# Optimization experiments

Measured on AMD Instinct MI355X. Metric: run time of the kernel, lower is better.

The kernel has to match this reference:

```python
import jax, jax.numpy as jnp
import numpy as np

N, S, T = 32, 256, 256
ENC, H, MEL, PRE, DIN, PN = 512, 256, 80, 128, 64, 512


def setup_inputs():
    key = jax.random.key(0)
    ks = iter(jax.random.split(key, 64))
    def rn(shape, s=0.05):
        return jax.random.normal(next(ks), shape, dtype=jnp.float32) * s
    return dict(
        encoder_outputs=rn((N, S, ENC), 1.0),
        mels=rn((N, MEL, T), 1.0),
        text_lengths=jax.random.randint(next(ks), (N,), 1, S),
        output_lengths=jax.random.randint(next(ks), (N,), 1, T),
        tf_ratio=0,
        enc_Wih=rn((2, 2, 4 * H, ENC)), enc_Whh=rn((2, 2, 4 * H, H)), enc_b=rn((2, 2, 4 * H)),
        Wk=rn((512, 512, 9)), bk=rn((512,)), Wv=rn((512, 512, 9)), bv=rn((512,)),
        Wq=rn((512, 64, 24)), bq=rn((512,)),
        initial_context=rn((1, 1, MEL), 1.0),
        pre_W1=rn((PRE, MEL), 0.1), pre_b1=rn((PRE,)), pre_s1=jnp.ones(PRE, jnp.float32),
        pre_W2=rn((PRE, PRE), 0.1), pre_b2=rn((PRE,)), pre_s2=jnp.ones(PRE, jnp.float32),
        pre_W3=rn((DIN, PRE), 0.1), pre_b3=rn((DIN,)),
        proj_W=rn((DIN, 512)), proj_b=rn((DIN,)),
        gamma=jnp.full((1,), 0.5, jnp.float32),
        dec_Wih0=rn((4 * H, DIN)), dec_Wih_rest=rn((3, 4 * H, H)), dec_Whh=rn((4, 4 * H, H)), dec_b=rn((4, 4 * H)),
        fc_W=rn((MEL, H), 0.1), fc_b=rn((MEL,)),
        stop_W=rn((1, 2 * H), 0.1), stop_b=rn((1,)),
        pn_W0=rn((PN, MEL, 5), 0.1), pn_b0=rn((PN,)),
        pn_Wmid=rn((3, PN, PN, 5)), pn_bmid=rn((3, PN)),
        pn_W4=rn((MEL, PN, 5)), pn_b4=rn((MEL,)),
        pn_bn_scale=jnp.ones((4, PN), jnp.float32), pn_bn_bias=jnp.zeros((4, PN), jnp.float32),
        pn_bn_scale_out=jnp.ones((MEL,), jnp.float32), pn_bn_bias_out=jnp.zeros((MEL,), jnp.float32),
        psine_w=jnp.ones((4, PN), jnp.float32),
    )


def _lstm_scan(xs, Wih, Whh, b, reverse=False):
    # xs: [T, N, D]; torch gate order (i, f, g, o); b = b_ih + b_hh combined
    n = xs.shape[1]
    h0 = jnp.zeros((n, Whh.shape[1]), xs.dtype)
    def step(carry, x):
        h, c = carry
        i, f, g, o = jnp.split(x @ Wih.T + h @ Whh.T + b, 4, axis=-1)
        c = jax.nn.sigmoid(f) * c + jax.nn.sigmoid(i) * jnp.tanh(g)
        h = jax.nn.sigmoid(o) * jnp.tanh(c)
        return (h, c), h
    (h, c), ys = jax.lax.scan(step, (h0, h0), xs, reverse=reverse)
    return ys, h, c


def _conv1d(x, w, b, pad):
    y = jax.lax.conv_general_dilated(x, w, (1,), [pad], dimension_numbers=('NCH', 'OIH', 'NCH'))
    return y + b[None, :, None]


def reference(encoder_outputs, mels, text_lengths, output_lengths, tf_ratio,
              enc_Wih, enc_Whh, enc_b, Wk, bk, Wv, bv, Wq, bq, initial_context,
              pre_W1, pre_b1, pre_s1, pre_W2, pre_b2, pre_s2, pre_W3, pre_b3,
              proj_W, proj_b, gamma, dec_Wih0, dec_Wih_rest, dec_Whh, dec_b,
              fc_W, fc_b, stop_W, stop_b, pn_W0, pn_b0, pn_Wmid, pn_bmid,
              pn_W4, pn_b4, pn_bn_scale, pn_bn_bias, pn_bn_scale_out, pn_bn_bias_out, psine_w):
    # ---- bidirectional 2-layer encoder LSTM ----
    x = encoder_outputs.transpose(1, 0, 2)  # [S, N, ENC]
    hs, cs = [], []
    for l in range(2):
        yf, hf, cf = _lstm_scan(x, enc_Wih[l, 0], enc_Whh[l, 0], enc_b[l, 0])
        yb, hb, cb = _lstm_scan(x, enc_Wih[l, 1], enc_Whh[l, 1], enc_b[l, 1], reverse=True)
        x = jnp.concatenate([yf, yb], -1)
        hs += [hf, hb]; cs += [cf, cb]
    h0 = jnp.stack(hs); c0 = jnp.stack(cs)      # [4, N, H]  (l0f,l0b,l1f,l1b)
    enc_fwd_hidden = hs[2]                       # hidden[-2] = layer1 forward
    enc_nct = x.transpose(1, 2, 0)               # [N, 512, S]
    # ---- K/V conv attention map ----
    k = _conv1d(enc_nct, Wk, bk, (0, 0))         # [N, 512, S-8]
    v = _conv1d(enc_nct, Wv, bv, (0, 0))
    a = jax.nn.softmax(jnp.einsum('nck,ndk->ncd', k, v), axis=-1)  # [N, 512, 512]
    # ---- teacher-forced inputs (tf_ratio == 0 -> rand(1) > 0 always) ----
    mels_ntc = mels.transpose(0, 2, 1)           # [N, T, MEL]
    nb, nt = mels_ntc.shape[0], mels_ntc.shape[1]
    teacher = jnp.concatenate([jnp.tile(initial_context, (nb, 1, 1)), mels_ntc], 1)[:, :nt]
    # prenet (eval: dropout off); PSine: sin(x) * w
    p = jnp.sin(teacher @ pre_W1.T + pre_b1) * pre_s1
    p = jnp.sin(p @ pre_W2.T + pre_b2) * pre_s2
    context = p @ pre_W3.T + pre_b3              # [N, T, 64]
    # ---- growing-context Q conv: at step i, output position i of the
    # kernel-24 pad-12 conv over context[:, :i+1] only involves kernel taps
    # 0..12 (taps 13..23 index positions > i which are zero padding), so it
    # equals a causal conv with the first 13 taps and left pad 12. ----
    q = _conv1d(context.transpose(0, 2, 1), Wq[:, :, :13], bq, (12, 0))  # [N, 512, T]
    o = jnp.einsum('ncd,ndt->ntc', a, q)         # [N, T, 512]
    dec_in = context + gamma * (o @ proj_W.T + proj_b)  # [N, T, 64]
    # ---- 4-layer decoder LSTM (eval: inter-layer dropout off) ----
    def dec_step(carry, xt):
        h, c = carry
        inp = xt
        nh, nc = [], []
        for l in range(4):
            Wih = dec_Wih0 if l == 0 else dec_Wih_rest[l - 1]
            i, f, g, oo = jnp.split(inp @ Wih.T + h[l] @ dec_Whh[l].T + dec_b[l], 4, axis=-1)
            cl = jax.nn.sigmoid(f) * c[l] + jax.nn.sigmoid(i) * jnp.tanh(g)
            hl = jax.nn.sigmoid(oo) * jnp.tanh(cl)
            nh.append(hl); nc.append(cl); inp = hl
        return (jnp.stack(nh), jnp.stack(nc)), inp
    _, top = jax.lax.scan(dec_step, (h0, c0), dec_in.transpose(1, 0, 2))  # [T, N, H]
    outputs = (top @ fc_W.T + fc_b).transpose(1, 2, 0)                    # [N, MEL, T]
    stop_in = jnp.concatenate([top, jnp.broadcast_to(enc_fwd_hidden, top.shape)], -1)
    stop_tokens = (stop_in @ stop_W.T + stop_b).transpose(1, 0, 2)        # [N, T, 1]
    # ---- postnet (eval: BN is per-channel affine, dropout off) ----
    y = _conv1d(outputs, pn_W0, pn_b0, (2, 2))
    y = jnp.sin(y * pn_bn_scale[0][None, :, None] + pn_bn_bias[0][None, :, None]) * psine_w[0][None, :, None]
    for i in range(3):
        y = _conv1d(y, pn_Wmid[i], pn_bmid[i], (2, 2))
        y = jnp.sin(y * pn_bn_scale[i + 1][None, :, None] + pn_bn_bias[i + 1][None, :, None]) * psine_w[i + 1][None, :, None]
    y = _conv1d(y, pn_W4, pn_b4, (2, 2))
    y = y * pn_bn_scale_out[None, :, None] + pn_bn_bias_out[None, :, None]
    post_preds = y + outputs
    return (outputs, post_preds, stop_tokens)
```

## Files before the change

### kernel.cpp

```cpp
#include <hip/hip_runtime.h>
#include <hip/hip_bf16.h>

typedef __hip_bfloat16 bf16;
#define DEV __device__ __forceinline__

typedef __attribute__((ext_vector_type(8))) short bfrag;
typedef __attribute__((ext_vector_type(4))) float facc;

#define PG_    0L
#define ABUF_  0L
#define DPG0_  8388608L
#define Y0_    16777216L
#define ENCT_  18874368L
#define KB_    20975872L
#define VB_    23073024L
#define ABF_   25170176L
#define TEA_   29364480L
#define P1_    29757696L
#define P2_    30281984L
#define CTXP_  30806272L
#define CTXL_  31080704L
#define QB_    31342848L
#define OB_    33440000L
#define DIN_   35537152L
#define TOP_   35799296L
#define OUTF_  36847872L
#define OUTT_  37503232L
#define PN1_   37902592L
#define PN2_   40032512L
#define WKT_   42162432L
#define WVT_   43342080L
#define WQT_   44521728L
#define W1P_   44734720L
#define PN0T_  44740864L
#define PNMT_  44863744L
#define PN4T_  46829824L
#define HDEC_  46964992L
#define HFIN_  47030528L
#define CFIN_  47063296L
#define FLAG_  47096320L
#define CVT_   47096336L
#define WS_NEED_BYTES (52092992L * 4L)

DEV float b2f(bf16 x) { return __bfloat162float(x); }
DEV bf16  f2b(float x) { return __float2bfloat16(x); }
DEV float flo(unsigned v) { union { unsigned u; float f; } c; c.u = v << 16; return c.f; }
DEV float fhi(unsigned v) { union { unsigned u; float f; } c; c.u = v & 0xffff0000u; return c.f; }
DEV unsigned bu(bf16 x) { union { bf16 b; unsigned short u; } c; c.b = x; return (unsigned)c.u; }
DEV unsigned pk2(float a, float b) { return bu(f2b(a)) | (bu(f2b(b)) << 16); }
DEV float sigm(float x) { return 1.0f / (1.0f + __expf(-x)); }

DEV void spin_ge(unsigned* f, unsigned tgt) {
  while (__hip_atomic_load(f, __ATOMIC_RELAXED, __HIP_MEMORY_SCOPE_AGENT) < tgt)
    __builtin_amdgcn_s_sleep(2);
}

DEV void acc8(float& a, uint4 w, const float* x) {
  a += flo(w.x) * x[0] + fhi(w.x) * x[1] + flo(w.y) * x[2] + fhi(w.y) * x[3]
     + flo(w.z) * x[4] + fhi(w.z) * x[5] + flo(w.w) * x[6] + fhi(w.w) * x[7];
}

__global__ void k_flag(const unsigned short* psw, unsigned* flag) {
  if (threadIdx.x == 0 && blockIdx.x == 0) *flag = (psw[0] != 0) ? 1u : 0u;
}

__global__ void k_cvt(const void* src, bf16* dst, long n, const unsigned* flag) {
  long i = (long)blockIdx.x * 256 + threadIdx.x;
  const long stride = (long)gridDim.x * 256;
  if (*flag) {
    const bf16* s = (const bf16*)src;
    for (; i < n; i += stride) dst[i] = s[i];
  } else {
    const float* s = (const float*)src;
    for (; i < n; i += stride) dst[i] = f2b(s[i]);
  }
}

enum { ACT_NONE = 0, ACT_BIAS = 1, ACT_PSINE = 2, ACT_POSTNET = 3, ACT_DECIN = 4, ACT_RESADD = 5 };
enum { SM_F32 = 0, SM_BF16 = 1, SM_PADROW = 2, SM_NCT = 3, SM_TNF32 = 4, SM_RESOUT = 5 };

struct GP {
  const bf16* A; const bf16* B;
  long az, bz, btap;
  int M, N, K, taps;
  int rshift, rpitch;
  float* Cf; bf16* Cb;
  long cz; int cld;
  int p2, pad2, tmax, tp;
  const bf16* bias; long biasz;
  const bf16* s1; const bf16* s2; const bf16* s3;
  const bf16* aux; int auxld;
  const bf16* gamma; const float* res;
};

template<int SM, int ACTM>
__global__ __launch_bounds__(256) void k_gemm(GP p) {
  __shared__ bf16 As[64][40];
  __shared__ bf16 Bs[64][40];
  const int tid = threadIdx.x;
  const int z = blockIdx.z;
  const bf16* Ab = p.A + (long)z * p.az;
  const bf16* Bb = p.B + (long)z * p.bz;
  const int m0 = blockIdx.x * 64, c0 = blockIdx.y * 64;
  const int w = tid >> 6, l = tid & 63;
  const int lrow = tid & 63, lk = (tid >> 6) * 8;
  facc acc[4];
  #pragma unroll
  for (int s = 0; s < 4; ++s) acc[s] = facc{0.f, 0.f, 0.f, 0.f};
  const int am = m0 + lrow;
  const int grp = am >> p.rshift;
  const long arowbase = (long)grp * p.rpitch + (am - (grp << p.rshift));
  const int brow = c0 + lrow;
  const bool bok = brow < p.N;
  const int arow_f = w * 16 + (l & 15);
  const int kf = (l >> 4) * 8;
  for (int j = 0; j < p.taps; ++j) {
    const bf16* Aj = Ab + (arowbase + j) * (long)p.K + lk;
    const bf16* Bj = Bb + (long)j * p.btap + (long)brow * p.K + lk;
    for (int k0 = 0; k0 < p.K; k0 += 32) {
      __syncthreads();
      {
        uint4 av = *(const uint4*)(Aj + k0);
        *(uint4*)&As[lrow][lk] = av;
        uint4 bvv; bvv.x = bvv.y = bvv.z = bvv.w = 0u;
        if (bok) bvv = *(const uint4*)(Bj + k0);
        *(uint4*)&Bs[lrow][lk] = bvv;
      }
      __syncthreads();
      bfrag af = *(const bfrag*)&As[arow_f][kf];
      #pragma unroll
      for (int s = 0; s < 4; ++s) {
        bfrag bf = *(const bfrag*)&Bs[s * 16 + (l & 15)][kf];
        acc[s] = __builtin_amdgcn_mfma_f32_16x16x32_bf16(af, bf, acc[s], 0, 0, 0);
      }
    }
  }
  float gf = 0.f;
  if constexpr (ACTM == ACT_DECIN) gf = b2f(p.gamma[0]);
  #pragma unroll
  for (int s = 0; s < 4; ++s) {
    const int c = c0 + s * 16 + (l & 15);
    if (c >= p.N) continue;
    #pragma unroll
    for (int i = 0; i < 4; ++i) {
      const int m = m0 + w * 16 + ((l >> 4) << 2) + i;
      const int n_ = m >> 8, t_ = m & 255;
      float x = acc[s][i];
      if constexpr (ACTM == ACT_BIAS) x += b2f(p.bias[(long)z * p.biasz + c]);
      else if constexpr (ACTM == ACT_PSINE) x = sinf(x + b2f(p.bias[c])) * b2f(p.s1[c]);
      else if constexpr (ACTM == ACT_POSTNET) x = sinf((x + b2f(p.bias[c])) * b2f(p.s1[c]) + b2f(p.s2[c])) * b2f(p.s3[c]);
      else if constexpr (ACTM == ACT_DECIN) x = b2f(p.aux[(long)m * p.auxld + c]) + gf * (x + b2f(p.bias[c]));
      else if constexpr (ACTM == ACT_RESADD) x = (x + b2f(p.bias[c])) * b2f(p.s1[c]) + b2f(p.s2[c]);
      if constexpr (SM == SM_F32) p.Cf[(long)z * p.cz + (long)m * p.cld + c] = x;
      else if constexpr (SM == SM_BF16) p.Cb[(long)z * p.cz + (long)m * p.cld + c] = f2b(x);
      else if constexpr (SM == SM_PADROW) p.Cb[((long)n_ * p.p2 + p.pad2 + t_) * (long)p.cld + c] = f2b(x);
      else if constexpr (SM == SM_NCT) { if (t_ < p.tmax) p.Cb[((long)n_ * p.p2 + c) * (long)p.tp + t_] = f2b(x); }
      else if constexpr (SM == SM_TNF32) { const int nn = m & 31, tt = m >> 5; p.Cf[((long)nn * p.p2 + c) * (long)p.tp + tt] = x; }
      else if constexpr (SM == SM_RESOUT) { const long off = ((long)n_ * p.p2 + c) * (long)p.tp + t_; p.Cf[off] = x + p.res[off]; }
    }
  }
}

__global__ void k_wtr2(const bf16* __restrict__ in, bf16* __restrict__ out) {
  long i = (long)blockIdx.x * 256 + threadIdx.x;
  if (i >= 524288L) return;
  int jj = (int)(i & 7);
  int r = (int)((i >> 3) & 1023);
  int k8 = (int)((i >> 13) & 31);
  int d = (int)(i >> 18);
  out[i] = in[((long)d * 1024 + r) * 256 + k8 * 8 + jj];
}

__global__ __launch_bounds__(256) void k_enc_scan(
    const float* __restrict__ pg,
    const bf16* __restrict__ WT,
    bf16* __restrict__ ycat,
    float* __restrict__ hfin, float* __restrict__ cfin,
    int layer)
{
  __shared__ float Hs[2][256];
  const int u = threadIdx.x;
  const int d = (int)(blockIdx.x >> 5);
  const int n = (int)(blockIdx.x & 31);
  const bf16* Wd = WT + (long)d * 32 * 1024 * 8;
  const float* pgn = pg + (long)(d * 32 + n) * 256 * 1024;
  float cst = 0.f;
  Hs[0][u] = 0.f;
  __syncthreads();
  for (int it = 0; it < 256; ++it) {
    const int s = d ? (255 - it) : it;
    const int par = it & 1;
    const float* pgs = pgn + (long)s * 1024;
    float a0 = pgs[u], a1 = pgs[256 + u], a2 = pgs[512 + u], a3 = pgs[768 + u];
    #pragma unroll 2
    for (int k8 = 0; k8 < 32; ++k8) {
      float x[8];
      *(float4*)&x[0] = *(const float4*)&Hs[par][k8 * 8];
      *(float4*)&x[4] = *(const float4*)&Hs[par][k8 * 8 + 4];
      const bf16* wb = Wd + ((long)k8 * 1024 + u) * 8;
      acc8(a0, *(const uint4*)(wb), x);
      acc8(a1, *(const uint4*)(wb + 2048), x);
      acc8(a2, *(const uint4*)(wb + 4096), x);
      acc8(a3, *(const uint4*)(wb + 6144), x);
    }
    cst = sigm(a1) * cst + sigm(a0) * tanhf(a2);
    float h = sigm(a3) * tanhf(cst);
    Hs[par ^ 1][u] = h;
    ycat[((long)n * 256 + s) * 512 + d * 256 + u] = f2b(h);
    if (it == 255) {
      hfin[((long)(layer * 2 + d) * 32 + n) * 256 + u] = h;
      cfin[((long)(layer * 2 + d) * 32 + n) * 256 + u] = cst;
    }
    __syncthreads();
  }
}

__global__ __launch_bounds__(256) void k_dec_scan(
    const float* __restrict__ dpg0,
    const bf16* __restrict__ Wih_rest,
    const bf16* __restrict__ Whh,
    const bf16* __restrict__ dec_b,
    unsigned* __restrict__ hdec,
    const float* __restrict__ cfin,
    bf16* __restrict__ top,
    unsigned* __restrict__ flags)
{
  __shared__ bf16 Wl[16][520];
  __shared__ bf16 XH[32][536];
  __shared__ float Gs[16 * 33];
  __shared__ float Hst[128];
  const int tid = threadIdx.x;
  const int layer = (int)(blockIdx.x >> 6);
  const int g = (int)(blockIdx.x & 63);
  const int u0 = g * 4;
  const int kstart = (layer == 0) ? 256 : 0;
  {
    const int r = tid >> 4, seg = tid & 15;
    const int grow = (r >> 2) * 256 + u0 + (r & 3);
    const int kk = seg * 32;
    const bool part0 = kk < 256;
    if (!(part0 && layer == 0)) {
      const bf16* wp = part0
          ? (Wih_rest + ((long)(layer - 1) * 1024 + grow) * 256 + kk)
          : (Whh + ((long)layer * 1024 + grow) * 256 + (kk - 256));
      for (int q = 0; q < 32; q += 8) {
        uint4 v = *(const uint4*)(wp + q);
        *(uint4*)&Wl[r][kk + q] = v;
      }
    }
  }
  const int pn = tid >> 2, pu = tid & 3;
  float cst = 0.f, bi0 = 0.f, bi1 = 0.f, bi2 = 0.f, bi3 = 0.f;
  if (tid < 128) {
    cst = cfin[((long)layer * 32 + pn) * 256 + u0 + pu];
    if (layer > 0) {
      bi0 = b2f(dec_b[layer * 1024 + u0 + pu]);
      bi1 = b2f(dec_b[layer * 1024 + 256 + u0 + pu]);
      bi2 = b2f(dec_b[layer * 1024 + 512 + u0 + pu]);
      bi3 = b2f(dec_b[layer * 1024 + 768 + u0 + pu]);
    }
  }
  __syncthreads();
  for (int t = 0; t < 256; ++t) {
    if (tid < 64) {
      if (layer > 0) spin_ge(&flags[((layer - 1) * 64 + tid) * 16], (unsigned)(t + 1));
    } else if (tid < 128) {
      if (t >= 1) spin_ge(&flags[(layer * 64 + (tid - 64)) * 16], (unsigned)t);
    } else if (tid < 192) {
      if (layer < 3 && t >= 2) spin_ge(&flags[((layer + 1) * 64 + (tid - 128)) * 16], (unsigned)(t - 1));
    }
    __syncthreads();
    const int rp = (t + layer + 1) & 1, wpar = (t + layer) & 1;
    {
      const int n = tid >> 3, seg = tid & 7;
      if (layer > 0 || seg >= 4) {
        const unsigned* src = (seg < 4)
            ? (hdec + (((long)(layer - 1) * 2 + rp) * 32 + n) * 128 + seg * 32)
            : (hdec + (((long)layer * 2 + rp) * 32 + n) * 128 + (seg - 4) * 32);
        const int base = seg * 64;
        #pragma unroll
        for (int q = 0; q < 32; q += 4) {
          unsigned long long v01 = __hip_atomic_load((const unsigned long long*)(src + q),
                                                     __ATOMIC_RELAXED, __HIP_MEMORY_SCOPE_AGENT);
          unsigned long long v23 = __hip_atomic_load((const unsigned long long*)(src + q + 2),
                                                     __ATOMIC_RELAXED, __HIP_MEMORY_SCOPE_AGENT);
          *(uint4*)&XH[n][base + q * 2] =
              make_uint4((unsigned)v01, (unsigned)(v01 >> 32), (unsigned)v23, (unsigned)(v23 >> 32));
        }
      }
    }
    __syncthreads();
    {
      const int r = tid & 15, n0 = (tid >> 4) * 2;
      float a0 = 0, a1 = 0;
      const bf16* wr = &Wl[r][0];
      const bf16* xa = &XH[n0][0];
      const bf16* xb = &XH[n0 + 1][0];
      #pragma unroll 4
      for (int k = kstart; k < 512; k += 4) {
        uint2 wv = *(const uint2*)(wr + k);
        uint2 va = *(const uint2*)(xa + k);
        uint2 vb = *(const uint2*)(xb + k);
        float w0 = flo(wv.x), w1 = fhi(wv.x), w2 = flo(wv.y), w3 = fhi(wv.y);
        a0 += w0 * flo(va.x) + w1 * fhi(va.x) + w2 * flo(va.y) + w3 * fhi(va.y);
        a1 += w0 * flo(vb.x) + w1 * fhi(vb.x) + w2 * flo(vb.y) + w3 * fhi(vb.y);
      }
      Gs[r * 33 + n0] = a0;
      Gs[r * 33 + n0 + 1] = a1;
    }
    __syncthreads();
    if (tid < 128) {
      float g0 = Gs[(0 * 4 + pu) * 33 + pn] + bi0;
      float g1 = Gs[(1 * 4 + pu) * 33 + pn] + bi1;
      float g2 = Gs[(2 * 4 + pu) * 33 + pn] + bi2;
      float g3 = Gs[(3 * 4 + pu) * 33 + pn] + bi3;
      if (layer == 0) {
        const float* pp = dpg0 + ((long)pn * 256 + t) * 1024;
        g0 += pp[u0 + pu]; g1 += pp[256 + u0 + pu];
        g2 += pp[512 + u0 + pu]; g3 += pp[768 + u0 + pu];
      }
      cst = sigm(g1) * cst + sigm(g0) * tanhf(g2);
      float h = sigm(g3) * tanhf(cst);
      Hst[tid] = h;
      if (layer == 3) top[((long)t * 32 + pn) * 256 + u0 + pu] = f2b(h);
    }
    __syncthreads();
    if (tid < 64) {
      const int hn = tid >> 1, pr = tid & 1;
      unsigned v = pk2(Hst[hn * 4 + pr * 2], Hst[hn * 4 + pr * 2 + 1]);
      __hip_atomic_store(&hdec[(((long)layer * 2 + wpar) * 32 + hn) * 128 + (u0 >> 1) + pr], v,
                         __ATOMIC_RELAXED, __HIP_MEMORY_SCOPE_AGENT);
    }
    asm volatile("s_waitcnt vmcnt(0)" ::: "memory");
    __syncthreads();
    if (tid == 0)
      __hip_atomic_store(&flags[(layer * 64 + g) * 16], (unsigned)(t + 1),
                         __ATOMIC_RELAXED, __HIP_MEMORY_SCOPE_AGENT);
  }
}

__global__ void k_wtr(const void* __restrict__ in, bf16* __restrict__ out,
                      int Cout, int Cin, int Cpad, int taps, int tstride, long total,
                      const unsigned* __restrict__ flag) {
  long i = (long)blockIdx.x * 256 + threadIdx.x;
  if (i >= total) return;
  int ci = (int)(i % Cpad); long r = i / Cpad; int co = (int)(r % Cout); int j = (int)(r / Cout);
  float v = 0.f;
  if (ci < Cin) {
    long idx = ((long)co * Cin + ci) * tstride + j;
    v = (*flag) ? b2f(((const bf16*)in)[idx]) : ((const float*)in)[idx];
  }
  out[i] = f2b(v);
}

__global__ void k_softmax(const float* __restrict__ raw, bf16* __restrict__ out) {
  __shared__ float red[256];
  const long row = blockIdx.x;
  const float* r = raw + row * 512;
  const int tid = threadIdx.x;
  float a = r[tid], b = r[tid + 256];
  red[tid] = fmaxf(a, b);
  __syncthreads();
  for (int s = 128; s > 0; s >>= 1) { if (tid < s) red[tid] = fmaxf(red[tid], red[tid + s]); __syncthreads(); }
  const float m = red[0];
  __syncthreads();
  float e0 = __expf(a - m), e1 = __expf(b - m);
  red[tid] = e0 + e1;
  __syncthreads();
  for (int s = 128; s > 0; s >>= 1) { if (tid < s) red[tid] += red[tid + s]; __syncthreads(); }
  const float inv = 1.f / red[0];
  out[row * 512 + tid] = f2b(e0 * inv);
  out[row * 512 + tid + 256] = f2b(e1 * inv);
}

__global__ void k_teacher(const bf16* __restrict__ mels, const bf16* __restrict__ ictx, bf16* __restrict__ out) {
  long i = (long)blockIdx.x * 256 + threadIdx.x;
  if (i >= 8192L * 96) return;
  int c = (int)(i % 96); long m = i / 96; int n = (int)(m >> 8), t = (int)(m & 255);
  float v = 0.f;
  if (c < 80) v = (t == 0) ? b2f(ictx[c]) : b2f(mels[((long)n * 80 + c) * 256 + (t - 1)]);
  out[i] = f2b(v);
}

__global__ void k_ctxcopy(const bf16* __restrict__ ctxp, bf16* __restrict__ ctxl) {
  long i = (long)blockIdx.x * 256 + threadIdx.x;
  if (i >= 8192L * 64) return;
  int c = (int)(i & 63); long m = i >> 6; int n = (int)(m >> 8), t = (int)(m & 255);
  ctxl[i] = ctxp[((long)n * 268 + 12 + t) * 64 + c];
}

__global__ void k_hdec_init(const float* __restrict__ hfin, unsigned* __restrict__ hdec) {
  int i = blockIdx.x * 256 + threadIdx.x;
  if (i >= 16384) return;
  int l = i >> 12, r = i & 4095;
  unsigned v = pk2(hfin[(long)l * 8192 + r * 2], hfin[(long)l * 8192 + r * 2 + 1]);
  hdec[((long)l * 2 + 0) * 4096 + r] = v;
  hdec[((long)l * 2 + 1) * 4096 + r] = v;
}

__global__ void k_outcopy1(const float* __restrict__ of, float* __restrict__ o) {
  long i = (long)blockIdx.x * 256 + threadIdx.x;
  if (i < 655360L) o[i] = of[i];
}

__global__ void k_outcopy2(const float* __restrict__ of, bf16* __restrict__ ot) {
  long i = (long)blockIdx.x * 256 + threadIdx.x;
  if (i >= 655360L) return;
  int c = (int)(i % 80); long m = i / 80; int n = (int)(m >> 8), t = (int)(m & 255);
  ot[((long)n * 260 + 2 + t) * 96 + c] = f2b(of[((long)n * 80 + c) * 256 + t]);
}

__global__ void k_stop(const bf16* __restrict__ top, const float* __restrict__ hfin,
                       const bf16* __restrict__ sW, const bf16* __restrict__ sb, float* __restrict__ out) {
  int i = blockIdx.x * 256 + threadIdx.x;
  if (i >= 8192) return;
  int n = i >> 8, t = i & 255;
  float acc = b2f(sb[0]);
  const bf16* tr = top + ((long)t * 32 + n) * 256;
  for (int h = 0; h < 256; ++h) acc += b2f(tr[h]) * b2f(sW[h]);
  const float* er = hfin + ((long)2 * 32 + n) * 256;
  for (int h = 0; h < 256; ++h) acc += er[h] * b2f(sW[256 + h]);
  out[(long)n * 256 + t] = acc;
}

extern "C" void kernel_launch(void* const* d_in, const int* in_sizes, int n_in,
                              void* d_out, int out_size, void* d_ws, size_t ws_size,
                              hipStream_t stream) {
  (void)in_sizes; (void)n_in; (void)out_size;
  if (ws_size < (size_t)WS_NEED_BYTES) return;

  float* ws = (float*)d_ws;
  float* out0 = (float*)d_out;
  float* out1 = out0 + 655360L;
  float* out2 = out0 + 1310720L;
  #define WF(off) (ws + (off))
  #define WB(off) ((bf16*)(ws + (off)))
  unsigned* flagp = (unsigned*)WF(FLAG_);

  hipMemsetAsync(WF(ENCT_), 0, 2101248L * 4, stream);
  hipMemsetAsync(WF(KB_), 0, 2097152L * 4, stream);
  hipMemsetAsync(WF(VB_), 0, 2097152L * 4, stream);
  hipMemsetAsync(WF(CTXP_), 0, 274432L * 4, stream);
  hipMemsetAsync(WF(OUTT_), 0, 399360L * 4, stream);

  k_flag<<<dim3(1), dim3(64), 0, stream>>>((const unsigned short*)d_in[44], flagp);
  bf16* cv[48] = {};
  {
    struct CvtEnt { int idx; long n; };
    static const CvtEnt cvts[] = {
      {0, 4194304}, {1, 655360}, {5, 2097152}, {6, 1048576}, {7, 4096},
      {9, 512}, {11, 512}, {13, 512}, {14, 80},
      {16, 128}, {17, 128}, {18, 16384}, {19, 128}, {20, 128}, {21, 8192}, {22, 64},
      {23, 32768}, {24, 64}, {25, 1},
      {26, 65536}, {27, 786432}, {28, 1048576}, {29, 4096},
      {30, 20480}, {31, 80}, {32, 512}, {33, 1},
      {35, 512}, {37, 1536}, {39, 80},
      {40, 2048}, {41, 2048}, {42, 80}, {43, 80}, {44, 2048},
    };
    bf16* arena = WB(CVT_);
    long pos = 0;
    for (const auto& c : cvts) {
      bf16* dst = arena + pos;
      long g = (c.n + 255) / 256; if (g > 2048) g = 2048;
      k_cvt<<<dim3((unsigned)g), dim3(256), 0, stream>>>(d_in[c.idx], dst, c.n, flagp);
      cv[c.idx] = dst;
      pos += (c.n + 15) & ~15L;
    }
  }

  const bf16* enc_out = cv[0];
  const bf16* mels    = cv[1];
  const bf16* eWih    = cv[5];
  const bf16* eWhh    = cv[6];
  const bf16* eb      = cv[7];
  const bf16* bk      = cv[9];
  const bf16* bv      = cv[11];
  const bf16* bq      = cv[13];
  const bf16* ictx    = cv[14];
  const bf16* pb1     = cv[16];
  const bf16* ps1     = cv[17];
  const bf16* pW2     = cv[18];
  const bf16* pb2     = cv[19];
  const bf16* ps2     = cv[20];
  const bf16* pW3     = cv[21];
  const bf16* pb3     = cv[22];
  const bf16* prW     = cv[23];
  const bf16* prb     = cv[24];
  const bf16* gam     = cv[25];
  const bf16* dWih0   = cv[26];
  const bf16* dWihr   = cv[27];
  const bf16* dWhh    = cv[28];
  const bf16* db      = cv[29];
  const bf16* fcW     = cv[30];
  const bf16* fcb     = cv[31];
  const bf16* sW      = cv[32];
  const bf16* sb      = cv[33];
  const bf16* pnb0    = cv[35];
  const bf16* pnbm    = cv[37];
  const bf16* pnb4    = cv[39];
  const bf16* bns     = cv[40];
  const bf16* bnb     = cv[41];
  const bf16* bnso    = cv[42];
  const bf16* bnbo    = cv[43];

  auto tr = [&](const void* in, bf16* o, int Cout, int Cin, int Cpad, int to, int ts) {
    long tot = (long)to * Cout * Cpad;
    k_wtr<<<dim3((unsigned)((tot + 255) / 256)), dim3(256), 0, stream>>>(in, o, Cout, Cin, Cpad, to, ts, tot, flagp);
  };
  tr(d_in[8],  WB(WKT_), 512, 512, 512, 9, 9);
  tr(d_in[10], WB(WVT_), 512, 512, 512, 9, 9);
  tr(d_in[12], WB(WQT_), 512, 64, 64, 13, 24);
  tr(d_in[15], WB(W1P_), 128, 80, 96, 1, 1);
  tr(d_in[34], WB(PN0T_), 512, 80, 96, 5, 5);
  tr(d_in[36], WB(PNMT_), 1536, 512, 512, 5, 5);
  tr(d_in[38], WB(PN4T_), 80, 512, 512, 5, 5);

  {
    GP p{}; p.A = enc_out; p.az = 0; p.rshift = 8; p.rpitch = 256;
    p.B = eWih; p.bz = 1024L * 512; p.btap = 0;
    p.M = 8192; p.N = 1024; p.K = 512; p.taps = 1;
    p.Cf = WF(PG_); p.cz = 8388608; p.cld = 1024; p.bias = eb; p.biasz = 1024;
    k_gemm<SM_F32, ACT_BIAS><<<dim3(128, 16, 2), dim3(256), 0, stream>>>(p);
  }
  k_wtr2<<<dim3(2048), dim3(256), 0, stream>>>(eWhh, WB(PN1_));
  k_enc_scan<<<dim3(64), dim3(256), 0, stream>>>(
      WF(PG_), WB(PN1_), WB(Y0_), WF(HFIN_), WF(CFIN_), 0);
  {
    GP p{}; p.A = WB(Y0_); p.az = 0; p.rshift = 8; p.rpitch = 256;
    p.B = eWih + 2L * 1024 * 512; p.bz = 1024L * 512; p.btap = 0;
    p.M = 8192; p.N = 1024; p.K = 512; p.taps = 1;
    p.Cf = WF(PG_); p.cz = 8388608; p.cld = 1024; p.bias = eb + 2048; p.biasz = 1024;
    k_gemm<SM_F32, ACT_BIAS><<<dim3(128, 16, 2), dim3(256), 0, stream>>>(p);
  }
  k_wtr2<<<dim3(2048), dim3(256), 0, stream>>>(eWhh + 2L * 1024 * 256, WB(PN2_));
  k_enc_scan<<<dim3(64), dim3(256), 0, stream>>>(
      WF(PG_), WB(PN2_), WB(ENCT_), WF(HFIN_), WF(CFIN_), 1);
  hipMemsetAsync(WF(PN1_), 0, 2129920L * 4, stream);
  hipMemsetAsync(WF(PN2_), 0, 2129920L * 4, stream);

  for (int kv = 0; kv < 2; ++kv) {
    GP p{}; p.A = WB(ENCT_); p.az = 0; p.rshift = 8; p.rpitch = 256;
    p.B = kv ? WB(WVT_) : WB(WKT_); p.bz = 0; p.btap = 512L * 512;
    p.M = 8192; p.N = 512; p.K = 512; p.taps = 9;
    p.Cb = kv ? WB(VB_) : WB(KB_); p.cz = 0; p.cld = 512;
    p.p2 = 512; p.tp = 256; p.tmax = 248; p.bias = kv ? bv : bk; p.biasz = 0;
    k_gemm<SM_NCT, ACT_BIAS><<<dim3(128, 8, 1), dim3(256), 0, stream>>>(p);
  }
  {
    GP p{}; p.A = WB(KB_); p.az = 512L * 256; p.rshift = 9; p.rpitch = 512;
    p.B = WB(VB_); p.bz = 512L * 256; p.btap = 0;
    p.M = 512; p.N = 512; p.K = 256; p.taps = 1;
    p.Cf = WF(ABUF_); p.cz = 262144; p.cld = 512;
    k_gemm<SM_F32, ACT_NONE><<<dim3(8, 8, 32), dim3(256), 0, stream>>>(p);
  }
  k_softmax<<<dim3(16384), dim3(256), 0, stream>>>(WF(ABUF_), WB(ABF_));

  k_teacher<<<dim3(3072), dim3(256), 0, stream>>>(mels, ictx, WB(TEA_));
  {
    GP p{}; p.A = WB(TEA_); p.az = 0; p.rshift = 8; p.rpitch = 256;
    p.B = WB(W1P_); p.bz = 0; p.btap = 0;
    p.M = 8192; p.N = 128; p.K = 96; p.taps = 1;
    p.Cb = WB(P1_); p.cz = 0; p.cld = 128; p.bias = pb1; p.s1 = ps1;
    k_gemm<SM_BF16, ACT_PSINE><<<dim3(128, 2, 1), dim3(256), 0, stream>>>(p);
  }
  {
    GP p{}; p.A = WB(P1_); p.az = 0; p.rshift = 8; p.rpitch = 256;
    p.B = pW2; p.bz = 0; p.btap = 0;
    p.M = 8192; p.N = 128; p.K = 128; p.taps = 1;
    p.Cb = WB(P2_); p.cz = 0; p.cld = 128; p.bias = pb2; p.s1 = ps2;
    k_gemm<SM_BF16, ACT_PSINE><<<dim3(128, 2, 1), dim3(256), 0, stream>>>(p);
  }
  {
    GP p{}; p.A = WB(P2_); p.az = 0; p.rshift = 8; p.rpitch = 256;
    p.B = pW3; p.bz = 0; p.btap = 0;
    p.M = 8192; p.N = 64; p.K = 128; p.taps = 1;
    p.Cb = WB(CTXP_); p.cz = 0; p.cld = 64; p.p2 = 268; p.pad2 = 12; p.bias = pb3; p.biasz = 0;
    k_gemm<SM_PADROW, ACT_BIAS><<<dim3(128, 1, 1), dim3(256), 0, stream>>>(p);
  }
  k_ctxcopy<<<dim3(2048), dim3(256), 0, stream>>>(WB(CTXP_), WB(CTXL_));

  {
    GP p{}; p.A = WB(CTXP_); p.az = 0; p.rshift = 8; p.rpitch = 268;
    p.B = WB(WQT_); p.bz = 0; p.btap = 512L * 64;
    p.M = 8192; p.N = 512; p.K = 64; p.taps = 13;
    p.Cb = WB(QB_); p.cz = 0; p.cld = 512; p.bias = bq; p.biasz = 0;
    k_gemm<SM_BF16, ACT_BIAS><<<dim3(128, 8, 1), dim3(256), 0, stream>>>(p);
  }
  {
    GP p{}; p.A = WB(QB_); p.az = 256L * 512; p.rshift = 8; p.rpitch = 256;
    p.B = WB(ABF_); p.bz = 512L * 512; p.btap = 0;
    p.M = 256; p.N = 512; p.K = 512; p.taps = 1;
    p.Cb = WB(OB_); p.cz = 256L * 512; p.cld = 512;
    k_gemm<SM_BF16, ACT_NONE><<<dim3(4, 8, 32), dim3(256), 0, stream>>>(p);
  }
  {
    GP p{}; p.A = WB(OB_); p.az = 0; p.rshift = 8; p.rpitch = 256;
    p.B = prW; p.bz = 0; p.btap = 0;
    p.M = 8192; p.N = 64; p.K = 512; p.taps = 1;
    p.Cb = WB(DIN_); p.cz = 0; p.cld = 64;
    p.bias = prb; p.aux = WB(CTXL_); p.auxld = 64; p.gamma = gam;
    k_gemm<SM_BF16, ACT_DECIN><<<dim3(128, 1, 1), dim3(256), 0, stream>>>(p);
  }
  {
    GP p{}; p.A = WB(DIN_); p.az = 0; p.rshift = 8; p.rpitch = 256;
    p.B = dWih0; p.bz = 0; p.btap = 0;
    p.M = 8192; p.N = 1024; p.K = 64; p.taps = 1;
    p.Cf = WF(DPG0_); p.cz = 0; p.cld = 1024; p.bias = db; p.biasz = 0;
    k_gemm<SM_F32, ACT_BIAS><<<dim3(128, 16, 1), dim3(256), 0, stream>>>(p);
  }
  hipMemsetAsync(WF(ABUF_), 0, 256 * 16 * 4, stream);
  k_hdec_init<<<dim3(64), dim3(256), 0, stream>>>(WF(HFIN_), (unsigned*)WF(HDEC_));
  k_dec_scan<<<dim3(256), dim3(256), 0, stream>>>(
      WF(DPG0_), dWihr, dWhh, db, (unsigned*)WF(HDEC_), WF(CFIN_), WB(TOP_), (unsigned*)WF(ABUF_));

  {
    GP p{}; p.A = WB(TOP_); p.az = 0; p.rshift = 8; p.rpitch = 256;
    p.B = fcW; p.bz = 0; p.btap = 0;
    p.M = 8192; p.N = 80; p.K = 256; p.taps = 1;
    p.Cf = WF(OUTF_); p.p2 = 80; p.tp = 256; p.bias = fcb; p.biasz = 0;
    k_gemm<SM_TNF32, ACT_BIAS><<<dim3(128, 2, 1), dim3(256), 0, stream>>>(p);
  }
  k_outcopy1<<<dim3(2560), dim3(256), 0, stream>>>(WF(OUTF_), out0);
  k_outcopy2<<<dim3(2560), dim3(256), 0, stream>>>(WF(OUTF_), WB(OUTT_));
  k_stop<<<dim3(32), dim3(256), 0, stream>>>(WB(TOP_), WF(HFIN_), sW, sb, out2);

  {
    GP p{}; p.A = WB(OUTT_); p.az = 0; p.rshift = 8; p.rpitch = 260;
    p.B = WB(PN0T_); p.bz = 0; p.btap = 512L * 96;
    p.M = 8192; p.N = 512; p.K = 96; p.taps = 5;
    p.Cb = WB(PN1_); p.cz = 0; p.cld = 512; p.p2 = 260; p.pad2 = 2;
    p.bias = pnb0; p.s1 = bns; p.s2 = bnb; p.s3 = cv[44];
    k_gemm<SM_PADROW, ACT_POSTNET><<<dim3(128, 8, 1), dim3(256), 0, stream>>>(p);
  }
  for (int s3 = 0; s3 < 3; ++s3) {
    GP p{}; p.A = (s3 & 1) ? WB(PN2_) : WB(PN1_); p.az = 0; p.rshift = 8; p.rpitch = 260;
    p.B = WB(PNMT_) + (long)s3 * 512 * 512; p.bz = 0; p.btap = 1536L * 512;
    p.M = 8192; p.N = 512; p.K = 512; p.taps = 5;
    p.Cb = (s3 & 1) ? WB(PN1_) : WB(PN2_); p.cz = 0; p.cld = 512; p.p2 = 260; p.pad2 = 2;
    p.bias = pnbm + s3 * 512; p.s1 = bns + (s3 + 1) * 512; p.s2 = bnb + (s3 + 1) * 512; p.s3 = cv[44] + (s3 + 1) * 512;
    k_gemm<SM_PADROW, ACT_POSTNET><<<dim3(128, 8, 1), dim3(256), 0, stream>>>(p);
  }
  {
    GP p{}; p.A = WB(PN2_); p.az = 0; p.rshift = 8; p.rpitch = 260;
    p.B = WB(PN4T_); p.bz = 0; p.btap = 80L * 512;
    p.M = 8192; p.N = 80; p.K = 512; p.taps = 5;
    p.Cf = out1; p.p2 = 80; p.tp = 256;
    p.bias = pnb4; p.s1 = bnso; p.s2 = bnbo; p.res = WF(OUTF_);
    k_gemm<SM_RESOUT, ACT_RESADD><<<dim3(128, 2, 1), dim3(256), 0, stream>>>(p);
  }
}
```

Baseline: 7.686 ms.

## Replace per-layer flag polling with a coordinator-block global barrier in decoder scan

Adds an extra coordinator workgroup that polls all 256 per-block progress flags and publishes a global round counter to 8 replicated flags. The decoder LSTM blocks now run in wavefront rounds (t = R - layer) and each waits on a single global flag from one thread, instead of 192 threads polling neighbour-layer flags every step. This is meant to cut the polling traffic and synchronisation latency of the 256-step scan, at the cost of a full-grid barrier each round plus three extra rounds. Spin sleep is also shortened.

```diff
diff --git a/kernel.cpp b/kernel.cpp
--- a/kernel.cpp
+++ b/kernel.cpp
@@ -52,7 +52,7 @@
 
 DEV void spin_ge(unsigned* f, unsigned tgt) {
   while (__hip_atomic_load(f, __ATOMIC_RELAXED, __HIP_MEMORY_SCOPE_AGENT) < tgt)
-    __builtin_amdgcn_s_sleep(2);
+    __builtin_amdgcn_s_sleep(1);
 }
 
 DEV void acc8(float& a, uint4 w, const float* x) {
@@ -225,11 +225,33 @@
     bf16* __restrict__ top,
     unsigned* __restrict__ flags)
 {
+  unsigned* gflag = flags + 256 * 32;
+  const int tid = threadIdx.x;
+  if (blockIdx.x == 256) {
+    if (tid < 64) {
+      for (int target = 1; target <= 259; ++target) {
+        for (;;) {
+          unsigned mn = 0xffffffffu;
+          #pragma unroll
+          for (int q = 0; q < 4; ++q) {
+            unsigned v = __hip_atomic_load(&flags[(tid * 4 + q) * 32],
+                                           __ATOMIC_RELAXED, __HIP_MEMORY_SCOPE_AGENT);
+            mn = mn < v ? mn : v;
+          }
+          if (__all(mn >= (unsigned)target)) break;
+          __builtin_amdgcn_s_sleep(1);
+        }
+        if (tid < 8)
+          __hip_atomic_store(&gflag[tid * 64], (unsigned)target,
+                             __ATOMIC_RELAXED, __HIP_MEMORY_SCOPE_AGENT);
+      }
+    }
+    return;
+  }
   __shared__ bf16 Wl[16][520];
   __shared__ bf16 XH[32][536];
   __shared__ float Gs[16 * 33];
   __shared__ float Hst[128];
-  const int tid = threadIdx.x;
   const int layer = (int)(blockIdx.x >> 6);
   const int g = (int)(blockIdx.x & 63);
   const int u0 = g * 4;
@@ -261,80 +283,81 @@
     }
   }
   __syncthreads();
-  for (int t = 0; t < 256; ++t) {
-    if (tid < 64) {
-      if (layer > 0) spin_ge(&flags[((layer - 1) * 64 + tid) * 16], (unsigned)(t + 1));
-    } else if (tid < 128) {
-      if (t >= 1) spin_ge(&flags[(layer * 64 + (tid - 64)) * 16], (unsigned)t);
-    } else if (tid < 192) {
-      if (layer < 3 && t >= 2) spin_ge(&flags[((layer + 1) * 64 + (tid - 128)) * 16], (unsigned)(t - 1));
-    }
-    __syncthreads();
-    const int rp = (t + layer + 1) & 1, wpar = (t + layer) & 1;
-    {
-      const int n = tid >> 3, seg = tid & 7;
-      if (layer > 0 || seg >= 4) {
-        const unsigned* src = (seg < 4)
-            ? (hdec + (((long)(layer - 1) * 2 + rp) * 32 + n) * 128 + seg * 32)
-            : (hdec + (((long)layer * 2 + rp) * 32 + n) * 128 + (seg - 4) * 32);
-        const int base = seg * 64;
-        #pragma unroll
-        for (int q = 0; q < 32; q += 4) {
-          unsigned long long v01 = __hip_atomic_load((const unsigned long long*)(src + q),
-                                                     __ATOMIC_RELAXED, __HIP_MEMORY_SCOPE_AGENT);
-          unsigned long long v23 = __hip_atomic_load((const unsigned long long*)(src + q + 2),
-                                                     __ATOMIC_RELAXED, __HIP_MEMORY_SCOPE_AGENT);
-          *(uint4*)&XH[n][base + q * 2] =
-              make_uint4((unsigned)v01, (unsigned)(v01 >> 32), (unsigned)v23, (unsigned)(v23 >> 32));
+  unsigned* myflag = &flags[blockIdx.x * 32];
+  unsigned* mygf = &gflag[(blockIdx.x & 7) * 64];
+  for (int R = 0; R < 259; ++R) {
+    if (R > 0) {
+      if (tid == 0) spin_ge(mygf, (unsigned)R);
+      __syncthreads();
+    }
+    const int t = R - layer;
+    if (t >= 0 && t < 256) {
+      const int rp = (R + 1) & 1, wpar = R & 1;
+      {
+        const int n = tid >> 3, seg = tid & 7;
+        if (layer > 0 || seg >= 4) {
+          const unsigned* src = (seg < 4)
+              ? (hdec + (((long)(layer - 1) * 2 + rp) * 32 + n) * 128 + seg * 32)
+              : (hdec + (((long)layer * 2 + rp) * 32 + n) * 128 + (seg - 4) * 32);
+          const int base = seg * 64;
+          #pragma unroll
+          for (int q = 0; q < 32; q += 4) {
+            unsigned long long v01 = __hip_atomic_load((const unsigned long long*)(src + q),
+                                                       __ATOMIC_RELAXED, __HIP_MEMORY_SCOPE_AGENT);
+            unsigned long long v23 = __hip_atomic_load((const unsigned long long*)(src + q + 2),
+                                                       __ATOMIC_RELAXED, __HIP_MEMORY_SCOPE_AGENT);
+            *(uint4*)&XH[n][base + q * 2] =
+                make_uint4((unsigned)v01, (unsigned)(v01 >> 32), (unsigned)v23, (unsigned)(v23 >> 32));
+          }
         }
       }
-    }
-    __syncthreads();
-    {
-      const int r = tid & 15, n0 = (tid >> 4) * 2;
-      float a0 = 0, a1 = 0;
-      const bf16* wr = &Wl[r][0];
-      const bf16* xa = &XH[n0][0];
-      const bf16* xb = &XH[n0 + 1][0];
-      #pragma unroll 4
-      for (int k = kstart; k < 512; k += 4) {
-        uint2 wv = *(const uint2*)(wr + k);
-        uint2 va = *(const uint2*)(xa + k);
-        uint2 vb = *(const uint2*)(xb + k);
-        float w0 = flo(wv.x), w1 = fhi(wv.x), w2 = flo(wv.y), w3 = fhi(wv.y);
-        a0 += w0 * flo(va.x) + w1 * fhi(va.x) + w2 * flo(va.y) + w3 * fhi(va.y);
-        a1 += w0 * flo(vb.x) + w1 * fhi(vb.x) + w2 * flo(vb.y) + w3 * fhi(vb.y);
-      }
-      Gs[r * 33 + n0] = a0;
-      Gs[r * 33 + n0 + 1] = a1;
-    }
-    __syncthreads();
-    if (tid < 128) {
-      float g0 = Gs[(0 * 4 + pu) * 33 + pn] + bi0;
-      float g1 = Gs[(1 * 4 + pu) * 33 + pn] + bi1;
-      float g2 = Gs[(2 * 4 + pu) * 33 + pn] + bi2;
-      float g3 = Gs[(3 * 4 + pu) * 33 + pn] + bi3;
-      if (layer == 0) {
-        const float* pp = dpg0 + ((long)pn * 256 + t) * 1024;
-        g0 += pp[u0 + pu]; g1 += pp[256 + u0 + pu];
-        g2 += pp[512 + u0 + pu]; g3 += pp[768 + u0 + pu];
-      }
-      cst = sigm(g1) * cst + sigm(g0) * tanhf(g2);
-      float h = sigm(g3) * tanhf(cst);
-      Hst[tid] = h;
-      if (layer == 3) top[((long)t * 32 + pn) * 256 + u0 + pu] = f2b(h);
-    }
-    __syncthreads();
-    if (tid < 64) {
-      const int hn = tid >> 1, pr = tid & 1;
-      unsigned v = pk2(Hst[hn * 4 + pr * 2], Hst[hn * 4 + pr * 2 + 1]);
-      __hip_atomic_store(&hdec[(((long)layer * 2 + wpar) * 32 + hn) * 128 + (u0 >> 1) + pr], v,
-                         __ATOMIC_RELAXED, __HIP_MEMORY_SCOPE_AGENT);
-    }
-    asm volatile("s_waitcnt vmcnt(0)" ::: "memory");
+      __syncthreads();
+      {
+        const int r = tid & 15, n0 = (tid >> 4) * 2;
+        float a0 = 0, a1 = 0;
+        const bf16* wr = &Wl[r][0];
+        const bf16* xa = &XH[n0][0];
+        const bf16* xb = &XH[n0 + 1][0];
+        #pragma unroll 4
+        for (int k = kstart; k < 512; k += 4) {
+          uint2 wv = *(const uint2*)(wr + k);
+          uint2 va = *(const uint2*)(xa + k);
+          uint2 vb = *(const uint2*)(xb + k);
+          float w0 = flo(wv.x), w1 = fhi(wv.x), w2 = flo(wv.y), w3 = fhi(wv.y);
+          a0 += w0 * flo(va.x) + w1 * fhi(va.x) + w2 * flo(va.y) + w3 * fhi(va.y);
+          a1 += w0 * flo(vb.x) + w1 * fhi(vb.x) + w2 * flo(vb.y) + w3 * fhi(vb.y);
+        }
+        Gs[r * 33 + n0] = a0;
+        Gs[r * 33 + n0 + 1] = a1;
+      }
+      __syncthreads();
+      if (tid < 128) {
+        float g0 = Gs[(0 * 4 + pu) * 33 + pn] + bi0;
+        float g1 = Gs[(1 * 4 + pu) * 33 + pn] + bi1;
+        float g2 = Gs[(2 * 4 + pu) * 33 + pn] + bi2;
+        float g3 = Gs[(3 * 4 + pu) * 33 + pn] + bi3;
+        if (layer == 0) {
+          const float* pp = dpg0 + ((long)pn * 256 + t) * 1024;
+          g0 += pp[u0 + pu]; g1 += pp[256 + u0 + pu];
+          g2 += pp[512 + u0 + pu]; g3 += pp[768 + u0 + pu];
+        }
+        cst = sigm(g1) * cst + sigm(g0) * tanhf(g2);
+        float h = sigm(g3) * tanhf(cst);
+        Hst[tid] = h;
+        if (layer == 3) top[((long)t * 32 + pn) * 256 + u0 + pu] = f2b(h);
+      }
+      __syncthreads();
+      if (tid < 64) {
+        const int hn = tid >> 1, pr = tid & 1;
+        unsigned v = pk2(Hst[hn * 4 + pr * 2], Hst[hn * 4 + pr * 2 + 1]);
+        __hip_atomic_store(&hdec[(((long)layer * 2 + wpar) * 32 + hn) * 128 + (u0 >> 1) + pr], v,
+                           __ATOMIC_RELAXED, __HIP_MEMORY_SCOPE_AGENT);
+      }
+      asm volatile("s_waitcnt vmcnt(0)" ::: "memory");
+    }
     __syncthreads();
     if (tid == 0)
-      __hip_atomic_store(&flags[(layer * 64 + g) * 16], (unsigned)(t + 1),
+      __hip_atomic_store(myflag, (unsigned)(R + 1),
                          __ATOMIC_RELAXED, __HIP_MEMORY_SCOPE_AGENT);
   }
 }
@@ -608,9 +631,9 @@
     p.Cf = WF(DPG0_); p.cz = 0; p.cld = 1024; p.bias = db; p.biasz = 0;
     k_gemm<SM_F32, ACT_BIAS><<<dim3(128, 16, 1), dim3(256), 0, stream>>>(p);
   }
-  hipMemsetAsync(WF(ABUF_), 0, 256 * 16 * 4, stream);
+  hipMemsetAsync(WF(ABUF_), 0, 40960, stream);
   k_hdec_init<<<dim3(64), dim3(256), 0, stream>>>(WF(HFIN_), (unsigned*)WF(HDEC_));
-  k_dec_scan<<<dim3(256), dim3(256), 0, stream>>>(
+  k_dec_scan<<<dim3(257), dim3(256), 0, stream>>>(
       WF(DPG0_), dWihr, dWhh, db, (unsigned*)WF(HDEC_), WF(CFIN_), WB(TOP_), (unsigned*)WF(ABUF_));
 
   {
```

Result: no change. 7.782 ms (+1.3%).
